# Optimization experiments

Hardware: AMD Instinct MI355X
Metric: run time of the kernel (lower is better)

The kernel has to match this reference:

```python
import jax, jax.numpy as jnp
import numpy as np

ALPHA = 0.01  # ELU slope from init kwargs


def setup_inputs() -> dict:
    key = jax.random.key(0)
    k1, k2, k3, k4, k5 = jax.random.split(key, 5)
    B, L, D_IN, D_ATT = 8, 2048, 256, 128
    context = jax.random.normal(k1, (B, L, D_IN), dtype=jnp.float32)
    query = jax.random.normal(k2, (B, L, D_IN), dtype=jnp.float32)
    query_mask = jax.random.randint(k3, (B, L), 0, 2, dtype=jnp.int32)
    # Linear(in_size, attention_size, bias=False) weights (stored as [in, out])
    W_in = jax.random.normal(k4, (D_IN, D_ATT), dtype=jnp.float32) * 0.05
    W_mem = jax.random.normal(k5, (D_IN, D_ATT), dtype=jnp.float32) * 0.05
    return {"context": context, "query": query, "W_in": W_in,
            "W_mem": W_mem, "query_mask": query_mask}


def reference(context, query, W_in, W_mem, query_mask):
    # VariationalDropout is identity at inference; Linear -> ELU(alpha=0.01)
    inp = jax.nn.elu(jnp.einsum('bld,df->blf', context, W_in), ALPHA)   # [B, Lc, Datt]
    mem = jax.nn.elu(jnp.einsum('bld,df->blf', query, W_mem), ALPHA)    # [B, Lq, Datt]
    scale = inp.shape[-1] ** 0.5
    logits = jnp.einsum('bcf,bqf->bcq', inp, mem) / scale               # [B, Lc, Lq]
    big = jnp.finfo(logits.dtype).max
    # mask_diag=True: kill diagonal (self) positions
    Lq = logits.shape[-1]
    eye = jnp.eye(Lq, dtype=bool)
    logits = jnp.where(eye[None, :, :], -big, logits)
    # masked_softmax over the query axis using query_mask [B, Lq]
    valid = (query_mask > 0)[:, None, :]                                # [B, 1, Lq]
    logits = jnp.where(valid, logits, -big)
    score = jax.nn.softmax(logits, axis=-1)                             # [B, Lc, Lq]
    return jnp.einsum('bcq,bqd->bcd', score, query)                     # [B, Lc, D_in]
```

## Files before the change

kernel.cpp:

```cpp
#include <hip/hip_runtime.h>
#include <math.h>

typedef short v4s __attribute__((ext_vector_type(4)));
typedef short v8s __attribute__((ext_vector_type(8)));
typedef float v4f __attribute__((ext_vector_type(4)));

#define L2E 1.4426950408889634f
#define INV_SCALE 0.08838834764831845f
#define SCL2 (INV_SCALE * L2E)

static __device__ __forceinline__ short f2bf(float x) {
    union { float f; unsigned u; } c; c.f = x;
    unsigned u = c.u;
    unsigned r = (u + 0x7fffu + ((u >> 16) & 1u)) >> 16;
    return (short)r;
}

typedef __attribute__((address_space(3))) void lds_vt;
typedef __attribute__((address_space(1))) const void gl_vt;
static __device__ __forceinline__ void gload_lds16(const void* g, void* l) {
    __builtin_amdgcn_global_load_lds((gl_vt*)g, (lds_vt*)l, 16, 0, 0);
}

__global__ __launch_bounds__(256) void k_pre(const float* __restrict__ ctx,
                                             const float* __restrict__ qry,
                                             const float* __restrict__ Win,
                                             const float* __restrict__ Wmem,
                                             const int* __restrict__ qmask,
                                             short* __restrict__ Qa,
                                             short* __restrict__ Ka,
                                             short* __restrict__ VaT,
                                             float* __restrict__ maskadd) {
    __shared__ __align__(16) char sbuf[128 * 132 * 2];
    int x = blockIdx.x;
    int tid = threadIdx.x;
    if (x < 512) {
        short* WtS = (short*)sbuf;
        int msel = x & 255, isel = x >> 8;
        const float* X = isel ? qry : ctx;
        const float* W = isel ? Wmem : Win;
        short* Y = isel ? Ka : Qa;

        int w = tid >> 6, lane = tid & 63;
        int ln = lane & 15, qd = lane >> 4;
        int m0 = msel * 64 + w * 16;
        v4f zero = {0.f, 0.f, 0.f, 0.f};
        v4f o[8];
#pragma unroll
        for (int i = 0; i < 8; ++i) o[i] = zero;

#pragma unroll 1
        for (int kh = 0; kh < 2; ++kh) {
            if (kh) __syncthreads();
#pragma unroll 8
            for (int i = 0; i < 64; ++i) {
                int id = i * 256 + tid;
                int k = id >> 7, fp = id & 127;
                WtS[fp * 132 + k] = f2bf(W[(kh * 128 + k) * 128 + fp]);
            }
            __syncthreads();
#pragma unroll
            for (int kk = 0; kk < 4; ++kk) {
                const float* xp = X + (size_t)(m0 + ln) * 256 + kh * 128 + kk * 32 + qd * 8;
                float4 x0 = *(const float4*)xp;
                float4 x1 = *(const float4*)(xp + 4);
                v8s a;
                a[0] = f2bf(x0.x); a[1] = f2bf(x0.y); a[2] = f2bf(x0.z); a[3] = f2bf(x0.w);
                a[4] = f2bf(x1.x); a[5] = f2bf(x1.y); a[6] = f2bf(x1.z); a[7] = f2bf(x1.w);
#pragma unroll
                for (int nt = 0; nt < 8; ++nt) {
                    v8s bfr = *(const v8s*)(WtS + (nt * 16 + ln) * 132 + kk * 32 + qd * 8);
                    o[nt] = __builtin_amdgcn_mfma_f32_16x16x32_bf16(a, bfr, o[nt], 0, 0, 0);
                }
            }
        }
#pragma unroll
        for (int nt = 0; nt < 8; ++nt) {
#pragma unroll
            for (int r = 0; r < 4; ++r) {
                float v = o[nt][r];
                v = v > 0.f ? v : 0.01f * (__expf(v) - 1.f);
                Y[(size_t)(m0 + qd * 4 + r) * 128 + nt * 16 + ln] = f2bf(v);
            }
        }
    } else {
        float (*tile)[65] = (float(*)[65])sbuf;
        int t = x - 512;
        int q0 = (t & 31) * 64, d0 = ((t >> 5) & 3) * 64, b = t >> 7;
        int c = tid & 63;
        int r4 = tid >> 6;
#pragma unroll
        for (int i = 0; i < 16; ++i) {
            int r = r4 + i * 4;
            tile[r][c] = qry[(size_t)(b * 2048 + q0 + r) * 256 + d0 + c];
        }
        __syncthreads();
        int g = c >> 3, j = c & 7;
#pragma unroll
        for (int i = 0; i < 16; ++i) {
            int d = r4 + i * 4;
            int cs = ((g ^ (d & 7)) << 3) | j;
            VaT[(size_t)(b * 256 + d0 + d) * 2048 + q0 + cs] = f2bf(tile[c][d]);
        }
        if (d0 == 0 && tid < 64) {
            int qq = b * 2048 + q0 + tid;
            maskadd[qq] = (qmask[qq] > 0) ? 0.f : -__builtin_inff();
        }
    }
}

template<int NSPLIT, bool DIRECT>
__global__ __launch_bounds__(256, 2) void k_attn(const short* __restrict__ Qa,
                                                 const short* __restrict__ Ka,
                                                 const short* __restrict__ VaT,
                                                 const float* __restrict__ maskadd,
                                                 float* __restrict__ Opart,
                                                 float* __restrict__ lpart,
                                                 float* __restrict__ out) {
    __shared__ __align__(16) short VaS[2][256 * 64];
    __shared__ __align__(16) short PS[64 * 64];
    __shared__ float lS[4 * 64];

    const int STEPS = 32 / NSPLIT;
    int blk = blockIdx.x;
    int b = blk & 7;
    int t = blk >> 3;
    int c0 = (t & 31) * 64;
    int sp = t >> 5;
    int kv0 = sp * (2048 / NSPLIT);

    int tid = threadIdx.x;
    int w = tid >> 6, lane = tid & 63, ln = lane & 15, qd = lane >> 4;

    const short* qbase = Qa + (size_t)(b * 2048) * 128;
    const short* kbase = Ka + (size_t)(b * 2048 + kv0 + w * 16 + ln) * 128 + qd * 8;
    const short* vbase = VaT + (size_t)(b * 256) * 2048;
    const float* mbase = maskadd + b * 2048 + kv0 + w * 16 + qd * 4;

    v8s qf[4][4];
#pragma unroll
    for (int ct = 0; ct < 4; ++ct) {
        const short* qp = qbase + (size_t)(c0 + ct * 16 + ln) * 128 + qd * 8;
#pragma unroll
        for (int kk = 0; kk < 4; ++kk) qf[ct][kk] = *(const v8s*)(qp + kk * 32);
    }

    v4f zero = {0.f, 0.f, 0.f, 0.f};
    v4f o[4][4];
#pragma unroll
    for (int i = 0; i < 4; ++i)
#pragma unroll
        for (int j = 0; j < 4; ++j) o[i][j] = zero;
    float lacc[4] = {0.f, 0.f, 0.f, 0.f};

    auto stageV = [&](int q0s, int buf) {
        short* base = &VaS[buf][0] + w * 4096;
#pragma unroll
        for (int j = 0; j < 8; ++j) {
            int U = (w * 8 + j) * 64 + lane;
            int d = U >> 3, cc = U & 7;
            gload_lds16(vbase + (size_t)d * 2048 + q0s + cc * 8,
                        base + j * 512);
        }
    };

    v8s kfA[4], kfB[4];
    float4 mkA, mkB;
    stageV(kv0, 0);
    asm volatile("" ::: "memory");
#pragma unroll
    for (int kk = 0; kk < 4; ++kk) kfA[kk] = *(const v8s*)(kbase + kk * 32);
    mkA = *(const float4*)(mbase);
    asm volatile("" ::: "memory");
    stageV(kv0 + 64, 1);

#define ATT_STEP(IT, KFC, MKC, KFN, MKN) do {                                  \
    int q0 = kv0 + (IT) * 64;                                                  \
    int itn = ((IT) + 1) & (STEPS - 1);                                        \
    int itn2 = ((IT) + 2) & (STEPS - 1);                                       \
    {              \
        const short* kp = kbase + (size_t)itn * 8192;                          \
        _Pragma("unroll")                                                      \
        for (int kk = 0; kk < 4; ++kk) KFN[kk] = *(const v8s*)(kp + kk * 32);  \
        MKN = *(const float4*)(mbase + itn * 64);                              \
    }                                                                          \
        \
    asm volatile("s_waitcnt vmcnt(13)" ::: "memory");                          \
    int kvb = q0 + w * 16 + qd * 4;                                            \
    _Pragma("unroll")                                                          \
    for (int ct = 0; ct < 4; ++ct) {                                           \
        v4f s = zero;                                                          \
        _Pragma("unroll")                                                      \
        for (int kk = 0; kk < 4; ++kk)                                         \
            s = __builtin_amdgcn_mfma_f32_16x16x32_bf16(KFC[kk], qf[ct][kk],   \
                                                        s, 0, 0, 0);           \
        int cg = c0 + ct * 16 + ln;                                            \
        v4s pw;                                                                \
        float ls = 0.f;                                                        \
        _Pragma("unroll")                                                      \
        for (int r = 0; r < 4; ++r) {                                          \
            float v = s[r] * SCL2 + (&MKC.x)[r];                               \
            if (kvb + r == cg) v = -__builtin_inff();                          \
            float p = exp2f(v);                                                \
            ls += p;                                                           \
            pw[r] = f2bf(p);                                                   \
        }                                                                      \
        lacc[ct] += ls;                                                        \
        int hs = ((w * 2 + (qd >> 1)) ^ (ln & 7));                             \
        *(v4s*)(PS + (ct * 16 + ln) * 64 + hs * 8 + (qd & 1) * 4) = pw;        \
    }                                                                          \
    asm volatile("s_waitcnt lgkmcnt(0)" ::: "memory");                         \
    __builtin_amdgcn_s_barrier();                               \
    const short* vs = &VaS[(IT) & 1][0];                                       \
    __builtin_amdgcn_s_setprio(1);                                             \
    _Pragma("unroll")                                                          \
    for (int kk2 = 0; kk2 < 2; ++kk2) {                                        \
        v8s pf[4], vf[4];                                                      \
        _Pragma("unroll")                                                      \
        for (int ct = 0; ct < 4; ++ct)                                         \
            pf[ct] = *(const v8s*)(PS + (ct * 16 + ln) * 64 +                  \
                                   (((kk2 * 4 + qd) ^ (ln & 7)) << 3));        \
        _Pragma("unroll")                                                      \
        for (int dt = 0; dt < 4; ++dt) {                                       \
            int d = w * 64 + dt * 16 + ln;                                     \
            vf[dt] = *(const v8s*)(vs + d * 64 +                               \
                                   (((kk2 * 4 + qd) ^ (ln & 7)) << 3));        \
        }                                                                      \
        _Pragma("unroll")                                                      \
        for (int ct = 0; ct < 4; ++ct)                                         \
            _Pragma("unroll")                                                  \
            for (int dt = 0; dt < 4; ++dt)                                     \
                o[ct][dt] = __builtin_amdgcn_mfma_f32_16x16x32_bf16(           \
                    pf[ct], vf[dt], o[ct][dt], 0, 0, 0);                       \
    }                                                                          \
    __builtin_amdgcn_s_setprio(0);                                             \
            \
    asm volatile("s_waitcnt lgkmcnt(0)" ::: "memory");                         \
    stageV(kv0 + itn2 * 64, (IT) & 1);                                         \
    __builtin_amdgcn_s_barrier();                \
} while (0)

#pragma unroll 1
    for (int it2 = 0; it2 < STEPS; it2 += 2) {
        ATT_STEP(it2, kfA, mkA, kfB, mkB);
        ATT_STEP(it2 + 1, kfB, mkB, kfA, mkA);
    }
#undef ATT_STEP

    __syncthreads();
#pragma unroll
    for (int ct = 0; ct < 4; ++ct) {
        float v = lacc[ct];
        v += __shfl_xor(v, 16);
        v += __shfl_xor(v, 32);
        if (qd == 0) lS[w * 64 + ct * 16 + ln] = v;
    }
    __syncthreads();

#pragma unroll
    for (int ct = 0; ct < 4; ++ct) {
        float4 l0 = *(const float4*)(lS + 0 * 64 + ct * 16 + qd * 4);
        float4 l1 = *(const float4*)(lS + 1 * 64 + ct * 16 + qd * 4);
        float4 l2 = *(const float4*)(lS + 2 * 64 + ct * 16 + qd * 4);
        float4 l3 = *(const float4*)(lS + 3 * 64 + ct * 16 + qd * 4);
        float lv[4];
#pragma unroll
        for (int r = 0; r < 4; ++r)
            lv[r] = (&l0.x)[r] + (&l1.x)[r] + (&l2.x)[r] + (&l3.x)[r];
        int rowg = b * 2048 + c0 + ct * 16 + qd * 4;
        if (DIRECT) {
#pragma unroll
            for (int r = 0; r < 4; ++r) {
                float inv = 1.f / lv[r];
#pragma unroll
                for (int dt = 0; dt < 4; ++dt)
                    out[(size_t)(rowg + r) * 256 + w * 64 + dt * 16 + ln] =
                        o[ct][dt][r] * inv;
            }
        } else {
            float* op = Opart + (size_t)sp * (16384 * 256);
#pragma unroll
            for (int r = 0; r < 4; ++r)
#pragma unroll
                for (int dt = 0; dt < 4; ++dt)
                    op[(size_t)(rowg + r) * 256 + w * 64 + dt * 16 + ln] = o[ct][dt][r];
            if (ln == 0)
                *(float4*)(lpart + sp * 16384 + rowg) =
                    make_float4(lv[0], lv[1], lv[2], lv[3]);
        }
    }
}

template<int NSPLIT>
__global__ __launch_bounds__(256) void k_combine(const float* __restrict__ Opart,
                                                 const float* __restrict__ lpart,
                                                 float* __restrict__ out) {
    int idx = blockIdx.x * 256 + threadIdx.x;
    int row = idx >> 6, d4 = (idx & 63) * 4;
    float L = 0.f;
    float4 acc = {0.f, 0.f, 0.f, 0.f};
#pragma unroll
    for (int s = 0; s < NSPLIT; ++s) {
        L += lpart[s * 16384 + row];
        float4 v = *(const float4*)(Opart + (size_t)s * (16384 * 256) + (size_t)row * 256 + d4);
        acc.x += v.x; acc.y += v.y; acc.z += v.z; acc.w += v.w;
    }
    float inv = 1.f / L;
    float4 res = {acc.x * inv, acc.y * inv, acc.z * inv, acc.w * inv};
    *(float4*)(out + (size_t)row * 256 + d4) = res;
}

extern "C" void kernel_launch(void* const* d_in, const int* in_sizes, int n_in,
                              void* d_out, int out_size, void* d_ws, size_t ws_size,
                              hipStream_t stream) {
    const float* ctx  = (const float*)d_in[0];
    const float* qry  = (const float*)d_in[1];
    const float* win  = (const float*)d_in[2];
    const float* wmem = (const float*)d_in[3];
    const int* qmask  = (const int*)d_in[4];
    float* out = (float*)d_out;

    char* ws = (char*)d_ws;
    short* Qa      = (short*)(ws);
    short* Ka      = (short*)(ws + (4u << 20));
    short* VaT     = (short*)(ws + (8u << 20));
    float* maskadd = (float*)(ws + (16u << 20));
    float* lpart   = (float*)(ws + (16u << 20) + 131072);
    float* Opart   = (float*)(ws + (18u << 20));

    k_pre<<<dim3(1536), 256, 0, stream>>>(ctx, qry, win, wmem, qmask,
                                          Qa, Ka, VaT, maskadd);

    const size_t base = 18u << 20, part = 16u << 20;
    if (ws_size >= base + 2 * part) {
        k_attn<2, false><<<dim3(512), 256, 0, stream>>>(Qa, Ka, VaT, maskadd,
                                                        Opart, lpart, out);
        k_combine<2><<<dim3(4096), 256, 0, stream>>>(Opart, lpart, out);
    } else {
        k_attn<1, true><<<dim3(256), 256, 0, stream>>>(Qa, Ka, VaT, maskadd,
                                                       Opart, lpart, out);
    }
}
```

Baseline: 153.1 us.

## Split KV range across two wave groups in one block, combine via LDS

Replaces the two-way KV split across separate blocks plus a global combine kernel with a single 512-thread block. Two 4-wave groups each process half of the keys and reduce their partial outputs and row sums through shared memory before writing the final normalized output. This removes the partial-output round trip to global memory and the extra kernel launch. The cost is double the LDS per block (two V buffers and two P tiles), which may reduce occupancy, and the sub-group barriers now synchronize all 8 waves.

```diff
diff --git a/kernel.cpp b/kernel.cpp
--- a/kernel.cpp
+++ b/kernel.cpp
@@ -109,33 +109,29 @@
     }
 }
 
-template<int NSPLIT, bool DIRECT>
-__global__ __launch_bounds__(256, 2) void k_attn(const short* __restrict__ Qa,
+__global__ __launch_bounds__(512, 2) void k_attn(const short* __restrict__ Qa,
                                                  const short* __restrict__ Ka,
                                                  const short* __restrict__ VaT,
                                                  const float* __restrict__ maskadd,
-                                                 float* __restrict__ Opart,
-                                                 float* __restrict__ lpart,
                                                  float* __restrict__ out) {
-    __shared__ __align__(16) short VaS[2][256 * 64];
-    __shared__ __align__(16) short PS[64 * 64];
-    __shared__ float lS[4 * 64];
-
-    const int STEPS = 32 / NSPLIT;
+    __shared__ __align__(16) short VaS[2][2][256 * 64];
+    __shared__ __align__(16) short PS[2][64 * 64];
+    __shared__ float lS[8 * 64];
+
+    const int STEPS = 16;
     int blk = blockIdx.x;
     int b = blk & 7;
-    int t = blk >> 3;
-    int c0 = (t & 31) * 64;
-    int sp = t >> 5;
-    int kv0 = sp * (2048 / NSPLIT);
+    int c0 = (blk >> 3) * 64;
 
     int tid = threadIdx.x;
     int w = tid >> 6, lane = tid & 63, ln = lane & 15, qd = lane >> 4;
+    int g = w >> 2, wl = w & 3;
+    int kv0 = g * 1024;
 
     const short* qbase = Qa + (size_t)(b * 2048) * 128;
-    const short* kbase = Ka + (size_t)(b * 2048 + kv0 + w * 16 + ln) * 128 + qd * 8;
+    const short* kbase = Ka + (size_t)(b * 2048 + kv0 + wl * 16 + ln) * 128 + qd * 8;
     const short* vbase = VaT + (size_t)(b * 256) * 2048;
-    const float* mbase = maskadd + b * 2048 + kv0 + w * 16 + qd * 4;
+    const float* mbase = maskadd + b * 2048 + kv0 + wl * 16 + qd * 4;
 
     v8s qf[4][4];
 #pragma unroll
@@ -154,10 +150,10 @@
     float lacc[4] = {0.f, 0.f, 0.f, 0.f};
 
     auto stageV = [&](int q0s, int buf) {
-        short* base = &VaS[buf][0] + w * 4096;
+        short* base = &VaS[g][buf][0] + wl * 4096;
 #pragma unroll
         for (int j = 0; j < 8; ++j) {
-            int U = (w * 8 + j) * 64 + lane;
+            int U = (wl * 8 + j) * 64 + lane;
             int d = U >> 3, cc = U & 7;
             gload_lds16(vbase + (size_t)d * 2048 + q0s + cc * 8,
                         base + j * 512);
@@ -186,7 +182,7 @@
     }                                                                          \
         \
     asm volatile("s_waitcnt vmcnt(13)" ::: "memory");                          \
-    int kvb = q0 + w * 16 + qd * 4;                                            \
+    int kvb = q0 + wl * 16 + qd * 4;                                           \
     _Pragma("unroll")                                                          \
     for (int ct = 0; ct < 4; ++ct) {                                           \
         v4f s = zero;                                                          \
@@ -206,23 +202,23 @@
             pw[r] = f2bf(p);                                                   \
         }                                                                      \
         lacc[ct] += ls;                                                        \
-        int hs = ((w * 2 + (qd >> 1)) ^ (ln & 7));                             \
-        *(v4s*)(PS + (ct * 16 + ln) * 64 + hs * 8 + (qd & 1) * 4) = pw;        \
+        int hs = ((wl * 2 + (qd >> 1)) ^ (ln & 7));                            \
+        *(v4s*)(&PS[g][0] + (ct * 16 + ln) * 64 + hs * 8 + (qd & 1) * 4) = pw; \
     }                                                                          \
     asm volatile("s_waitcnt lgkmcnt(0)" ::: "memory");                         \
     __builtin_amdgcn_s_barrier();                               \
-    const short* vs = &VaS[(IT) & 1][0];                                       \
+    const short* vs = &VaS[g][(IT) & 1][0];                                    \
     __builtin_amdgcn_s_setprio(1);                                             \
     _Pragma("unroll")                                                          \
     for (int kk2 = 0; kk2 < 2; ++kk2) {                                        \
         v8s pf[4], vf[4];                                                      \
         _Pragma("unroll")                                                      \
         for (int ct = 0; ct < 4; ++ct)                                         \
-            pf[ct] = *(const v8s*)(PS + (ct * 16 + ln) * 64 +                  \
+            pf[ct] = *(const v8s*)(&PS[g][0] + (ct * 16 + ln) * 64 +           \
                                    (((kk2 * 4 + qd) ^ (ln & 7)) << 3));        \
         _Pragma("unroll")                                                      \
         for (int dt = 0; dt < 4; ++dt) {                                       \
-            int d = w * 64 + dt * 16 + ln;                                     \
+            int d = wl * 64 + dt * 16 + ln;                                    \
             vf[dt] = *(const v8s*)(vs + d * 64 +                               \
                                    (((kk2 * 4 + qd) ^ (ln & 7)) << 3));        \
         }                                                                      \
@@ -247,7 +243,9 @@
     }
 #undef ATT_STEP
 
+    asm volatile("s_waitcnt vmcnt(0)" ::: "memory");
     __syncthreads();
+
 #pragma unroll
     for (int ct = 0; ct < 4; ++ct) {
         float v = lacc[ct];
@@ -255,59 +253,46 @@
         v += __shfl_xor(v, 32);
         if (qd == 0) lS[w * 64 + ct * 16 + ln] = v;
     }
+
+    float* OS = (float*)&VaS[0][0][0];
+    if (g == 1) {
+#pragma unroll
+        for (int ct = 0; ct < 4; ++ct)
+#pragma unroll
+            for (int r = 0; r < 4; ++r)
+#pragma unroll
+                for (int dt = 0; dt < 4; ++dt)
+                    OS[(ct * 16 + qd * 4 + r) * 260 + wl * 64 + dt * 16 + ln] =
+                        o[ct][dt][r];
+    }
     __syncthreads();
 
-#pragma unroll
-    for (int ct = 0; ct < 4; ++ct) {
-        float4 l0 = *(const float4*)(lS + 0 * 64 + ct * 16 + qd * 4);
-        float4 l1 = *(const float4*)(lS + 1 * 64 + ct * 16 + qd * 4);
-        float4 l2 = *(const float4*)(lS + 2 * 64 + ct * 16 + qd * 4);
-        float4 l3 = *(const float4*)(lS + 3 * 64 + ct * 16 + qd * 4);
-        float lv[4];
-#pragma unroll
-        for (int r = 0; r < 4; ++r)
-            lv[r] = (&l0.x)[r] + (&l1.x)[r] + (&l2.x)[r] + (&l3.x)[r];
-        int rowg = b * 2048 + c0 + ct * 16 + qd * 4;
-        if (DIRECT) {
+    if (g == 0) {
+#pragma unroll
+        for (int ct = 0; ct < 4; ++ct) {
+            float lv[4];
+#pragma unroll
+            for (int r = 0; r < 4; ++r) {
+                float s = 0.f;
+#pragma unroll
+                for (int wv = 0; wv < 8; ++wv)
+                    s += lS[wv * 64 + ct * 16 + qd * 4 + r];
+                lv[r] = s;
+            }
+            int rowg = b * 2048 + c0 + ct * 16 + qd * 4;
 #pragma unroll
             for (int r = 0; r < 4; ++r) {
                 float inv = 1.f / lv[r];
 #pragma unroll
-                for (int dt = 0; dt < 4; ++dt)
-                    out[(size_t)(rowg + r) * 256 + w * 64 + dt * 16 + ln] =
-                        o[ct][dt][r] * inv;
-            }
-        } else {
-            float* op = Opart + (size_t)sp * (16384 * 256);
-#pragma unroll
-            for (int r = 0; r < 4; ++r)
-#pragma unroll
-                for (int dt = 0; dt < 4; ++dt)
-                    op[(size_t)(rowg + r) * 256 + w * 64 + dt * 16 + ln] = o[ct][dt][r];
-            if (ln == 0)
-                *(float4*)(lpart + sp * 16384 + rowg) =
-                    make_float4(lv[0], lv[1], lv[2], lv[3]);
-        }
-    }
-}
-
-template<int NSPLIT>
-__global__ __launch_bounds__(256) void k_combine(const float* __restrict__ Opart,
-                                                 const float* __restrict__ lpart,
-                                                 float* __restrict__ out) {
-    int idx = blockIdx.x * 256 + threadIdx.x;
-    int row = idx >> 6, d4 = (idx & 63) * 4;
-    float L = 0.f;
-    float4 acc = {0.f, 0.f, 0.f, 0.f};
-#pragma unroll
-    for (int s = 0; s < NSPLIT; ++s) {
-        L += lpart[s * 16384 + row];
-        float4 v = *(const float4*)(Opart + (size_t)s * (16384 * 256) + (size_t)row * 256 + d4);
-        acc.x += v.x; acc.y += v.y; acc.z += v.z; acc.w += v.w;
-    }
-    float inv = 1.f / L;
-    float4 res = {acc.x * inv, acc.y * inv, acc.z * inv, acc.w * inv};
-    *(float4*)(out + (size_t)row * 256 + d4) = res;
+                for (int dt = 0; dt < 4; ++dt) {
+                    int col = wl * 64 + dt * 16 + ln;
+                    float sum = o[ct][dt][r] +
+                                OS[(ct * 16 + qd * 4 + r) * 260 + col];
+                    out[(size_t)(rowg + r) * 256 + col] = sum * inv;
+                }
+            }
+        }
+    }
 }
 
 extern "C" void kernel_launch(void* const* d_in, const int* in_sizes, int n_in,
@@ -325,19 +310,8 @@
     short* Ka      = (short*)(ws + (4u << 20));
     short* VaT     = (short*)(ws + (8u << 20));
     float* maskadd = (float*)(ws + (16u << 20));
-    float* lpart   = (float*)(ws + (16u << 20) + 131072);
-    float* Opart   = (float*)(ws + (18u << 20));
 
     k_pre<<<dim3(1536), 256, 0, stream>>>(ctx, qry, win, wmem, qmask,
                                           Qa, Ka, VaT, maskadd);
-
-    const size_t base = 18u << 20, part = 16u << 20;
-    if (ws_size >= base + 2 * part) {
-        k_attn<2, false><<<dim3(512), 256, 0, stream>>>(Qa, Ka, VaT, maskadd,
-                                                        Opart, lpart, out);
-        k_combine<2><<<dim3(4096), 256, 0, stream>>>(Opart, lpart, out);
-    } else {
-        k_attn<1, true><<<dim3(256), 256, 0, stream>>>(Qa, Ka, VaT, maskadd,
-                                                       Opart, lpart, out);
-    }
-}
+    k_attn<<<dim3(256), 512, 0, stream>>>(Qa, Ka, VaT, maskadd, out);
+}
```

Result: no change. 151.1 us (-1.3%).
